# Kernel tuning notes

Hardware: AMD Instinct MI355X
Metric: run time of the kernel (lower is better)

## Reference

```python
import jax, jax.numpy as jnp
import numpy as np

N, E, F, H, A = 100000, 1600000, 256, 32, 64


def setup_inputs() -> dict:
    key = jax.random.key(0)
    ks = jax.random.split(key, 14)
    s = lambda k, shp, scale: (jax.random.normal(k, shp, dtype=jnp.float32) * scale)
    return {
        "features": jax.random.normal(ks[0], (N, F), dtype=jnp.float32),
        "edge_index": jax.random.randint(ks[1], (2, E), 0, N, dtype=jnp.int64),
        "W1": s(ks[2], (F, H), 1.0 / np.sqrt(F)), "b1": jnp.zeros((H,), jnp.float32),
        "W2": s(ks[3], (H, H), 1.0 / np.sqrt(H)), "b2": jnp.zeros((H,), jnp.float32),
        "pW1": s(ks[4], (H, 512), 1.0 / np.sqrt(H)), "pb1": jnp.zeros((512,), jnp.float32),
        "pW2": s(ks[5], (512, A), 1.0 / np.sqrt(512)), "pb2": jnp.zeros((A,), jnp.float32),
        "vW1": s(ks[6], (H, 512), 1.0 / np.sqrt(H)), "vb1": jnp.zeros((512,), jnp.float32),
        "vW2": s(ks[7], (512, 1), 1.0 / np.sqrt(512)), "vb2": jnp.zeros((1,), jnp.float32),
    }


def _gcn_conv(x, src, dst, W, b, n):
    # PyG GCNConv: x' = D^{-1/2} (A+I) D^{-1/2} (x W) + b  (self-loops already in src/dst)
    x = x @ W  # [n, out]
    deg = jax.ops.segment_sum(jnp.ones(src.shape[0], x.dtype), dst, num_segments=n)
    dinv = jnp.where(deg > 0, jax.lax.rsqrt(jnp.maximum(deg, 1e-12)), 0.0).astype(x.dtype)
    norm = dinv[src] * dinv[dst]                       # [E+n]
    msg = x[src] * norm[:, None]                       # gather + scale
    return jax.ops.segment_sum(msg, dst, num_segments=n) + b  # scatter-add


def reference(features, edge_index, W1, b1, W2, b2, pW1, pb1, pW2, pb2, vW1, vb1, vW2, vb2):
    n = features.shape[0]
    loop = jnp.arange(n, dtype=edge_index.dtype)
    src = jnp.concatenate([edge_index[0], loop])
    dst = jnp.concatenate([edge_index[1], loop])
    h = jax.nn.relu(_gcn_conv(features, src, dst, W1, b1, n))
    h = jax.nn.relu(_gcn_conv(h, src, dst, W2, b2, n))  # [n, H] == conv_out
    policy = jax.nn.relu(h @ pW1 + pb1) @ pW2 + pb2     # [n, A]
    value = jax.nn.relu(h @ vW1 + vb1) @ vW2 + vb2      # [n, 1]
    return policy, value
```

## Files before the change

### kernel.cpp

```cpp
#include <hip/hip_runtime.h>

#define FDIM 256
#define HDIM 32
#define D1   512
#define ADIM 64
#define BKT_SHIFT 9
#define BKT_NODES 512
#define CAP 12288

typedef __bf16 bf16x8 __attribute__((ext_vector_type(8)));
typedef float  f32x4  __attribute__((ext_vector_type(4)));

__device__ __forceinline__ float bf2f(unsigned short h){
  unsigned int u = ((unsigned int)h) << 16;
  return __builtin_bit_cast(float, u);
}
__device__ __forceinline__ unsigned short f2bf(float f){
  unsigned int u = __builtin_bit_cast(unsigned int, f);
  u = u + 0x7fff + ((u >> 16) & 1u);
  return (unsigned short)(u >> 16);
}
__device__ __forceinline__ unsigned int pk2(float a, float b){
  unsigned int ua = __builtin_bit_cast(unsigned int, a) + 0x8000u;
  unsigned int ub = __builtin_bit_cast(unsigned int, b) + 0x8000u;
  return (ua >> 16) | (ub & 0xffff0000u);
}

__global__ void k_zero(int* bkcur){
  bkcur[threadIdx.x] = 0;
}

__global__ __launch_bounds__(256) void k_stage(const int* __restrict__ src,
                                               const int* __restrict__ dst,
                                               int* __restrict__ bkcur,
                                               uint2* __restrict__ stage, int e){
  __shared__ int h[256], base[256], cur[256];
  int t = threadIdx.x;
  h[t] = 0; cur[t] = 0;
  __syncthreads();
  int lo = blockIdx.x*8192, hi = min(e, lo + 8192);
  for (int i = lo + t; i < hi; i += 256)
    atomicAdd(&h[dst[i] >> BKT_SHIFT], 1);
  __syncthreads();
  if (h[t] > 0) base[t] = t*CAP + atomicAdd(&bkcur[t], h[t]);
  __syncthreads();
  for (int i = lo + t; i < hi; i += 256){
    int d = dst[i]; int b = d >> BKT_SHIFT;
    int r = atomicAdd(&cur[b], 1);
    int idx = base[b] + r;
    if (idx < (b+1)*CAP)
      stage[idx] = make_uint2((unsigned)src[i], (unsigned)d);
  }
}

__global__ __launch_bounds__(256) void k_fine(const uint2* __restrict__ stage,
                                              const int* __restrict__ bkcur,
                                              int* __restrict__ rowptr,
                                              int* __restrict__ rowend,
                                              int* __restrict__ col,
                                              float* __restrict__ dinv, int n){
  __shared__ int h[512], ofs[512], s[256];
  int b = blockIdx.x, t = threadIdx.x;
  int e0 = b*CAP;
  int cnt = min(bkcur[b], CAP);
  int nb0 = b << BKT_SHIFT;
  h[t] = 0; h[t+256] = 0; __syncthreads();
  for (int i = e0 + t; i < e0 + cnt; i += 256)
    atomicAdd(&h[(int)stage[i].y - nb0], 1);
  __syncthreads();
  int a0 = h[2*t], a1 = h[2*t+1];
  int p0 = (a0 + 7) & ~7, p1 = (a1 + 7) & ~7;
  int v = p0 + p1;
  s[t] = v; __syncthreads();
  for (int off = 1; off < 256; off <<= 1){
    int tv = (t >= off) ? s[t-off] : 0; __syncthreads();
    s[t] += tv; __syncthreads();
  }
  int ex = s[t] - v;
  ofs[2*t] = ex; ofs[2*t+1] = ex + p0;
  int node0 = nb0 + 2*t, node1 = node0 + 1;
  if (node0 < n){
    rowptr[node0] = e0 + ex;       rowend[node0] = e0 + ex + p0;
    dinv[node0] = rsqrtf((float)(a0 + 1));
  }
  if (node1 < n){
    rowptr[node1] = e0 + ex + p0;  rowend[node1] = e0 + ex + p0 + p1;
    dinv[node1] = rsqrtf((float)(a1 + 1));
  }
  __syncthreads();
  for (int i = e0 + t; i < e0 + cnt; i += 256){
    uint2 u = stage[i];
    int r = atomicAdd(&ofs[(int)u.y - nb0], 1);
    col[e0 + r] = (int)u.x;
  }
  __syncthreads();
  {
    int st0 = ofs[2*t];
    for (int j = st0; j < ex + p0; ++j) col[e0 + j] = n;
    int st1 = ofs[2*t+1];
    for (int j = st1; j < ex + p0 + p1; ++j) col[e0 + j] = n;
  }
}

__device__ __forceinline__ void prep_one(int i, const float* __restrict__ src,
                                         unsigned short* __restrict__ dst,
                                         int nnt, int ld, int ncols){
  int j = i & 7; int L = (i >> 3) & 63; int t = i >> 9;
  int nt = t % nnt; int kb = t / nnt;
  int k = kb*32 + ((L >> 4) * 8) + j;
  int n = nt*16 + (L & 15);
  float v = (n < ncols) ? src[k*ld + n] : 0.f;
  dst[i] = f2bf(v);
}

__global__ void k_prep(const float* W1, const float* W2, const float* pW1,
                       const float* vW1, const float* pW2,
                       unsigned short* W1P, unsigned short* W2P, unsigned short* pW1P,
                       unsigned short* vW1P, unsigned short* pW2P){
  int i = blockIdx.x*256 + threadIdx.x;
  if (i < 8192) { prep_one(i, W1,  W1P,  2, 32, 32);   return; } i -= 8192;
  if (i < 1024) { prep_one(i, W2,  W2P,  2, 32, 32);   return; } i -= 1024;
  if (i < 16384){ prep_one(i, pW1, pW1P, 32, 512, 512); return; } i -= 16384;
  if (i < 16384){ prep_one(i, vW1, vW1P, 32, 512, 512); return; } i -= 16384;
  if (i < 32768){ prep_one(i, pW2, pW2P, 4, 64, 64);   return; }
}

__global__ __launch_bounds__(256) void k_gemm1(const float* __restrict__ feat,
                                               const unsigned short* __restrict__ W1P,
                                               const float* __restrict__ dinv,
                                               unsigned short* __restrict__ x1, int n){
  int lane = threadIdx.x & 63; int wv = threadIdx.x >> 6;
  int lid = lane & 15, quad = lane >> 4;
  int base = (blockIdx.x*4 + wv) * 16;
  int row = base + lid; if (row >= n) row = n - 1;
  const float* fr = feat + (size_t)row * FDIM;
  f32x4 acc0 = {0.f,0.f,0.f,0.f}, acc1 = {0.f,0.f,0.f,0.f};
#pragma unroll
  for (int kb = 0; kb < 8; ++kb){
    float4 fa = *(const float4*)(fr + kb*32 + quad*8);
    float4 fb = *(const float4*)(fr + kb*32 + quad*8 + 4);
    bf16x8 bfr;
    bfr[0]=(__bf16)fa.x; bfr[1]=(__bf16)fa.y; bfr[2]=(__bf16)fa.z; bfr[3]=(__bf16)fa.w;
    bfr[4]=(__bf16)fb.x; bfr[5]=(__bf16)fb.y; bfr[6]=(__bf16)fb.z; bfr[7]=(__bf16)fb.w;
    bf16x8 w0 = *(const bf16x8*)(W1P + (size_t)((kb*2+0)*64 + lane)*8);
    bf16x8 w1 = *(const bf16x8*)(W1P + (size_t)((kb*2+1)*64 + lane)*8);
    acc0 = __builtin_amdgcn_mfma_f32_16x16x32_bf16(w0, bfr, acc0, 0,0,0);
    acc1 = __builtin_amdgcn_mfma_f32_16x16x32_bf16(w1, bfr, acc1, 0,0,0);
  }
  int orow = base + lid;
  if (orow <= n){
    float di = (orow < n) ? dinv[orow] : 0.f;
    unsigned short* o = x1 + (size_t)orow*HDIM;
    uint2 q0, q1;
    q0.x = f2bf(acc0[0]*di) | ((unsigned)f2bf(acc0[1]*di)<<16);
    q0.y = f2bf(acc0[2]*di) | ((unsigned)f2bf(acc0[3]*di)<<16);
    q1.x = f2bf(acc1[0]*di) | ((unsigned)f2bf(acc1[1]*di)<<16);
    q1.y = f2bf(acc1[2]*di) | ((unsigned)f2bf(acc1[3]*di)<<16);
    *(uint2*)(o + quad*4)      = q0;
    *(uint2*)(o + 16 + quad*4) = q1;
  }
}

__global__ __launch_bounds__(256) void k_conv(const unsigned short* __restrict__ x,
                                              const float* __restrict__ dinv,
                                              const int* __restrict__ rowptr,
                                              const int* __restrict__ rowend,
                                              const int* __restrict__ col,
                                              const float* __restrict__ bias,
                                              unsigned short* __restrict__ y, int n){
  int node = (blockIdx.x*256 + threadIdx.x) >> 6;
  if (node >= n) return;
  int lane = threadIdx.x & 63;
  int c = lane & 31, eh = lane >> 5;
  float acc = (eh == 0) ? bf2f(x[(size_t)node*HDIM + c]) : 0.f;
  int rp = rowptr[node], re = rowend[node];
  int nb8 = (re - rp) >> 3;
  int jb = rp + (eh << 2);
#pragma clang loop unroll_count(2)
  for (int t = 0; t < nb8; ++t, jb += 8){
    int c0 = col[jb+0], c1 = col[jb+1], c2 = col[jb+2], c3 = col[jb+3];
    float v0 = bf2f(x[(size_t)c0*HDIM + c]);
    float v1 = bf2f(x[(size_t)c1*HDIM + c]);
    float v2 = bf2f(x[(size_t)c2*HDIM + c]);
    float v3 = bf2f(x[(size_t)c3*HDIM + c]);
    acc += (v0 + v1) + (v2 + v3);
  }
  acc += __shfl_xor(acc, 32);
  if (eh == 0){
    float v = acc * dinv[node] + bias[c];
    y[(size_t)node*HDIM + c] = f2bf(fmaxf(v, 0.f));
  }
}

__global__ __launch_bounds__(256) void k_gemm2(const unsigned short* __restrict__ h1,
                                               const unsigned short* __restrict__ W2P,
                                               const float* __restrict__ dinv,
                                               unsigned short* __restrict__ x2, int n){
  int lane = threadIdx.x & 63; int wv = threadIdx.x >> 6;
  int lid = lane & 15, quad = lane >> 4;
  int base = (blockIdx.x*4 + wv) * 16;
  int row = base + lid; if (row >= n) row = n - 1;
  bf16x8 hb = *(const bf16x8*)(h1 + (size_t)row*HDIM + quad*8);
  bf16x8 w0 = *(const bf16x8*)(W2P + (size_t)(0*64 + lane)*8);
  bf16x8 w1 = *(const bf16x8*)(W2P + (size_t)(1*64 + lane)*8);
  f32x4 z = {0.f,0.f,0.f,0.f};
  f32x4 a0 = __builtin_amdgcn_mfma_f32_16x16x32_bf16(w0, hb, z, 0,0,0);
  f32x4 a1 = __builtin_amdgcn_mfma_f32_16x16x32_bf16(w1, hb, z, 0,0,0);
  int orow = base + lid;
  if (orow <= n){
    float di = (orow < n) ? dinv[orow] : 0.f;
    unsigned short* o = x2 + (size_t)orow*HDIM;
    uint2 q0, q1;
    q0.x = f2bf(a0[0]*di) | ((unsigned)f2bf(a0[1]*di)<<16);
    q0.y = f2bf(a0[2]*di) | ((unsigned)f2bf(a0[3]*di)<<16);
    q1.x = f2bf(a1[0]*di) | ((unsigned)f2bf(a1[1]*di)<<16);
    q1.y = f2bf(a1[2]*di) | ((unsigned)f2bf(a1[3]*di)<<16);
    *(uint2*)(o + quad*4)      = q0;
    *(uint2*)(o + 16 + quad*4) = q1;
  }
}

#define TSTR 56
__global__ __launch_bounds__(256, 4) void k_head(const unsigned short* __restrict__ h,
    const unsigned short* __restrict__ pW1P, const unsigned short* __restrict__ pW2P,
    const unsigned short* __restrict__ vW1P, const float* __restrict__ vW2,
    const float* __restrict__ pb1, const float* __restrict__ pb2,
    const float* __restrict__ vb1, const float* __restrict__ vb2,
    float* __restrict__ pol, float* __restrict__ val, int n){
  __shared__ unsigned short lds[4*2*16*TSTR];
  int lane = threadIdx.x & 63; int wv = threadIdx.x >> 6;
  int lid = lane & 15, quad = lane >> 4;
  int nbase = (blockIdx.x*4 + wv) * 32;
  unsigned short* tb0 = lds + wv*(2*16*TSTR);
  unsigned short* tb1 = tb0 + 16*TSTR;
  int r0 = nbase + lid;      if (r0 >= n) r0 = n - 1;
  int r1 = nbase + 16 + lid; if (r1 >= n) r1 = n - 1;
  bf16x8 hf0 = *(const bf16x8*)(h + (size_t)r0*HDIM + quad*8);
  bf16x8 hf1 = *(const bf16x8*)(h + (size_t)r1*HDIM + quad*8);
  f32x4 z = {0.f,0.f,0.f,0.f};
  f32x4 acc[8] = {z,z,z,z,z,z,z,z};

#pragma unroll 2
  for (int kb = 0; kb < 16; ++kb){
    bf16x8 w0 = *(const bf16x8*)(pW1P + (size_t)((2*kb+0)*64 + lane)*8);
    bf16x8 w1 = *(const bf16x8*)(pW1P + (size_t)((2*kb+1)*64 + lane)*8);
    f32x4 c00 = __builtin_amdgcn_mfma_f32_16x16x32_bf16(w0, hf0, z, 0,0,0);
    f32x4 c01 = __builtin_amdgcn_mfma_f32_16x16x32_bf16(w1, hf0, z, 0,0,0);
    f32x4 c10 = __builtin_amdgcn_mfma_f32_16x16x32_bf16(w0, hf1, z, 0,0,0);
    f32x4 c11 = __builtin_amdgcn_mfma_f32_16x16x32_bf16(w1, hf1, z, 0,0,0);
    float4 b0 = *(const float4*)(pb1 + (2*kb+0)*16 + quad*4);
    float4 b1 = *(const float4*)(pb1 + (2*kb+1)*16 + quad*4);
    uint2 q;
    q.x = pk2(fmaxf(c00[0]+b0.x,0.f), fmaxf(c00[1]+b0.y,0.f));
    q.y = pk2(fmaxf(c00[2]+b0.z,0.f), fmaxf(c00[3]+b0.w,0.f));
    *(uint2*)(tb0 + lid*TSTR + quad*4) = q;
    q.x = pk2(fmaxf(c01[0]+b1.x,0.f), fmaxf(c01[1]+b1.y,0.f));
    q.y = pk2(fmaxf(c01[2]+b1.z,0.f), fmaxf(c01[3]+b1.w,0.f));
    *(uint2*)(tb0 + lid*TSTR + 16 + quad*4) = q;
    q.x = pk2(fmaxf(c10[0]+b0.x,0.f), fmaxf(c10[1]+b0.y,0.f));
    q.y = pk2(fmaxf(c10[2]+b0.z,0.f), fmaxf(c10[3]+b0.w,0.f));
    *(uint2*)(tb1 + lid*TSTR + quad*4) = q;
    q.x = pk2(fmaxf(c11[0]+b1.x,0.f), fmaxf(c11[1]+b1.y,0.f));
    q.y = pk2(fmaxf(c11[2]+b1.z,0.f), fmaxf(c11[3]+b1.w,0.f));
    *(uint2*)(tb1 + lid*TSTR + 16 + quad*4) = q;
    bf16x8 a0 = *(const bf16x8*)(tb0 + lid*TSTR + quad*8);
    bf16x8 a1 = *(const bf16x8*)(tb1 + lid*TSTR + quad*8);
#pragma unroll
    for (int tt = 0; tt < 4; ++tt){
      bf16x8 b = *(const bf16x8*)(pW2P + (size_t)((kb*4+tt)*64 + lane)*8);
      acc[tt]   = __builtin_amdgcn_mfma_f32_16x16x32_bf16(a0, b, acc[tt],   0,0,0);
      acc[4+tt] = __builtin_amdgcn_mfma_f32_16x16x32_bf16(a1, b, acc[4+tt], 0,0,0);
    }
  }
#pragma unroll
  for (int g = 0; g < 2; ++g){
#pragma unroll
    for (int tt = 0; tt < 4; ++tt){
      float pb2v = pb2[tt*16 + lid];
#pragma unroll
      for (int r = 0; r < 4; ++r){
        int node = nbase + g*16 + quad*4 + r;
        if (node < n) pol[(size_t)node*ADIM + tt*16 + lid] = acc[g*4+tt][r] + pb2v;
      }
    }
  }

  float va0 = 0.f, va1 = 0.f;
#pragma unroll 4
  for (int t = 0; t < 32; ++t){
    bf16x8 a = *(const bf16x8*)(vW1P + (size_t)(t*64 + lane)*8);
    f32x4 c0 = __builtin_amdgcn_mfma_f32_16x16x32_bf16(a, hf0, z, 0,0,0);
    f32x4 c1 = __builtin_amdgcn_mfma_f32_16x16x32_bf16(a, hf1, z, 0,0,0);
    float4 b  = *(const float4*)(vb1 + t*16 + quad*4);
    float4 w2 = *(const float4*)(vW2 + t*16 + quad*4);
    va0 += fmaxf(c0[0]+b.x,0.f)*w2.x + fmaxf(c0[1]+b.y,0.f)*w2.y
         + fmaxf(c0[2]+b.z,0.f)*w2.z + fmaxf(c0[3]+b.w,0.f)*w2.w;
    va1 += fmaxf(c1[0]+b.x,0.f)*w2.x + fmaxf(c1[1]+b.y,0.f)*w2.y
         + fmaxf(c1[2]+b.z,0.f)*w2.z + fmaxf(c1[3]+b.w,0.f)*w2.w;
  }
  va0 += __shfl_xor(va0, 16); va0 += __shfl_xor(va0, 32);
  va1 += __shfl_xor(va1, 16); va1 += __shfl_xor(va1, 32);
  if (quad == 0){
    float vb = vb2[0];
    int n0 = nbase + lid, n1 = nbase + 16 + lid;
    if (n0 < n) val[n0] = va0 + vb;
    if (n1 < n) val[n1] = va1 + vb;
  }
}

extern "C" void kernel_launch(void* const* d_in, const int* in_sizes, int n_in,
                              void* d_out, int out_size, void* d_ws, size_t ws_size,
                              hipStream_t stream){
  const float* feat = (const float*)d_in[0];
  const int*   edge = (const int*)d_in[1];
  const float* W1  = (const float*)d_in[2];
  const float* b1  = (const float*)d_in[3];
  const float* W2  = (const float*)d_in[4];
  const float* b2  = (const float*)d_in[5];
  const float* pW1 = (const float*)d_in[6];
  const float* pb1 = (const float*)d_in[7];
  const float* pW2 = (const float*)d_in[8];
  const float* pb2 = (const float*)d_in[9];
  const float* vW1 = (const float*)d_in[10];
  const float* vb1 = (const float*)d_in[11];
  const float* vW2 = (const float*)d_in[12];
  const float* vb2 = (const float*)d_in[13];
  int n = in_sizes[0] / FDIM;
  int e = in_sizes[1] / 2;
  int nbk = (n + BKT_NODES - 1) >> BKT_SHIFT;

  char* w = (char*)d_ws;
  auto alloc = [&](size_t bytes)->char*{
    char* p = w; w += (bytes + 255) & ~(size_t)255; return p;
  };
  size_t nodebuf = (size_t)(n+1)*HDIM*2;
  size_t stagesz = (size_t)nbk*CAP*8;
  char* stagebuf = alloc(stagesz > 2*nodebuf ? stagesz : 2*nodebuf);
  uint2* stage = (uint2*)stagebuf;
  unsigned short* x1 = (unsigned short*)stagebuf;
  unsigned short* h1 = (unsigned short*)(stagebuf + nodebuf);
  int*   col    = (int*)  alloc((size_t)nbk*CAP*4);
  int*   rowptr = (int*)  alloc((size_t)n*4);
  int*   rowend = (int*)  alloc((size_t)n*4);
  float* dinv   = (float*)alloc((size_t)n*4);
  int*   bkcur  = (int*)  alloc(256*4);
  unsigned short* W1P  = (unsigned short*)alloc(8192*2);
  unsigned short* W2P  = (unsigned short*)alloc(1024*2);
  unsigned short* pW1P = (unsigned short*)alloc(16384*2);
  unsigned short* vW1P = (unsigned short*)alloc(16384*2);
  unsigned short* pW2P = (unsigned short*)alloc(32768*2);

  int gb  = (n + 63)/64;
  int hb2 = (n + 127)/128;

  k_zero <<<1, 256, 0, stream>>>(bkcur);
  k_stage<<<(e + 8191)/8192, 256, 0, stream>>>(edge, edge + e, bkcur, stage, e);
  k_fine <<<nbk, 256, 0, stream>>>(stage, bkcur, rowptr, rowend, col, dinv, n);
  k_prep <<<(74752 + 255)/256, 256, 0, stream>>>(W1, W2, pW1, vW1, pW2,
                                                 W1P, W2P, pW1P, vW1P, pW2P);
  k_gemm1<<<gb, 256, 0, stream>>>(feat, W1P, dinv, x1, n);
  k_conv <<<(n + 3)/4, 256, 0, stream>>>(x1, dinv, rowptr, rowend, col, b1, h1, n);
  k_gemm2<<<gb, 256, 0, stream>>>(h1, W2P, dinv, x1, n);
  k_conv <<<(n + 3)/4, 256, 0, stream>>>(x1, dinv, rowptr, rowend, col, b2, h1, n);
  float* pol = (float*)d_out;
  float* val = pol + (size_t)n*ADIM;
  k_head <<<hb2, 256, 0, stream>>>(h1, pW1P, pW2P, vW1P, vW2,
                                   pb1, pb2, vb1, vb2, pol, val, n);
}
```

Baseline: 370.4 us.

## Fuse W2 GEMM into first conv, pack staged edges, merge zero into prep

The second-layer dense transform (h1 @ W2, scaled by dinv) now runs inside the first aggregation kernel. W2 sits in LDS and each node's post-ReLU row goes through a small per-wave LDS dot product, so the separate MFMA gemm2 kernel and its h1 round-trip through global memory are gone. Staged edges are packed into one 32-bit word (local dst in the high bits, src in the low 17 bits), which halves staging traffic. The bucket-counter zeroing is folded into the weight-prep kernel to save a launch, and the row bounds are clamped to CAP. The risks are that the fused GEMM uses scalar FP32 FMAs instead of MFMA, adds an LDS barrier to each conv block, and the 17-bit packing limits src to fewer than 131072 nodes.

```diff
diff --git a/kernel.cpp b/kernel.cpp
--- a/kernel.cpp
+++ b/kernel.cpp
@@ -26,14 +26,34 @@
   return (ua >> 16) | (ub & 0xffff0000u);
 }
 
-__global__ void k_zero(int* bkcur){
-  bkcur[threadIdx.x] = 0;
+__device__ __forceinline__ void prep_one(int i, const float* __restrict__ src,
+                                         unsigned short* __restrict__ dst,
+                                         int nnt, int ld, int ncols){
+  int j = i & 7; int L = (i >> 3) & 63; int t = i >> 9;
+  int nt = t % nnt; int kb = t / nnt;
+  int k = kb*32 + ((L >> 4) * 8) + j;
+  int n = nt*16 + (L & 15);
+  float v = (n < ncols) ? src[k*ld + n] : 0.f;
+  dst[i] = f2bf(v);
+}
+
+__global__ void k_prep(const float* W1, const float* pW1, const float* vW1,
+                       const float* pW2,
+                       unsigned short* W1P, unsigned short* pW1P,
+                       unsigned short* vW1P, unsigned short* pW2P,
+                       int* bkcur){
+  int i = blockIdx.x*256 + threadIdx.x;
+  if (i < 256)  { bkcur[i] = 0;                          return; } i -= 256;
+  if (i < 8192) { prep_one(i, W1,  W1P,  2, 32, 32);     return; } i -= 8192;
+  if (i < 16384){ prep_one(i, pW1, pW1P, 32, 512, 512);  return; } i -= 16384;
+  if (i < 16384){ prep_one(i, vW1, vW1P, 32, 512, 512);  return; } i -= 16384;
+  if (i < 32768){ prep_one(i, pW2, pW2P, 4, 64, 64);     return; }
 }
 
 __global__ __launch_bounds__(256) void k_stage(const int* __restrict__ src,
                                                const int* __restrict__ dst,
                                                int* __restrict__ bkcur,
-                                               uint2* __restrict__ stage, int e){
+                                               unsigned int* __restrict__ stage, int e){
   __shared__ int h[256], base[256], cur[256];
   int t = threadIdx.x;
   h[t] = 0; cur[t] = 0;
@@ -49,11 +69,11 @@
     int r = atomicAdd(&cur[b], 1);
     int idx = base[b] + r;
     if (idx < (b+1)*CAP)
-      stage[idx] = make_uint2((unsigned)src[i], (unsigned)d);
-  }
-}
-
-__global__ __launch_bounds__(256) void k_fine(const uint2* __restrict__ stage,
+      stage[idx] = ((unsigned int)(d & (BKT_NODES-1)) << 17) | (unsigned int)src[i];
+  }
+}
+
+__global__ __launch_bounds__(256) void k_fine(const unsigned int* __restrict__ stage,
                                               const int* __restrict__ bkcur,
                                               int* __restrict__ rowptr,
                                               int* __restrict__ rowend,
@@ -66,7 +86,7 @@
   int nb0 = b << BKT_SHIFT;
   h[t] = 0; h[t+256] = 0; __syncthreads();
   for (int i = e0 + t; i < e0 + cnt; i += 256)
-    atomicAdd(&h[(int)stage[i].y - nb0], 1);
+    atomicAdd(&h[stage[i] >> 17], 1);
   __syncthreads();
   int a0 = h[2*t], a1 = h[2*t+1];
   int p0 = (a0 + 7) & ~7, p1 = (a1 + 7) & ~7;
@@ -80,49 +100,26 @@
   ofs[2*t] = ex; ofs[2*t+1] = ex + p0;
   int node0 = nb0 + 2*t, node1 = node0 + 1;
   if (node0 < n){
-    rowptr[node0] = e0 + ex;       rowend[node0] = e0 + ex + p0;
+    rowptr[node0] = e0 + ex;       rowend[node0] = e0 + min(ex + p0, CAP);
     dinv[node0] = rsqrtf((float)(a0 + 1));
   }
   if (node1 < n){
-    rowptr[node1] = e0 + ex + p0;  rowend[node1] = e0 + ex + p0 + p1;
+    rowptr[node1] = e0 + min(ex + p0, CAP);  rowend[node1] = e0 + min(ex + p0 + p1, CAP);
     dinv[node1] = rsqrtf((float)(a1 + 1));
   }
   __syncthreads();
   for (int i = e0 + t; i < e0 + cnt; i += 256){
-    uint2 u = stage[i];
-    int r = atomicAdd(&ofs[(int)u.y - nb0], 1);
-    col[e0 + r] = (int)u.x;
+    unsigned int u = stage[i];
+    int r = atomicAdd(&ofs[(int)(u >> 17)], 1);
+    if (r < CAP) col[e0 + r] = (int)(u & 0x1FFFF);
   }
   __syncthreads();
   {
     int st0 = ofs[2*t];
-    for (int j = st0; j < ex + p0; ++j) col[e0 + j] = n;
+    for (int j = st0; j < ex + p0 && j < CAP; ++j) col[e0 + j] = n;
     int st1 = ofs[2*t+1];
-    for (int j = st1; j < ex + p0 + p1; ++j) col[e0 + j] = n;
-  }
-}
-
-__device__ __forceinline__ void prep_one(int i, const float* __restrict__ src,
-                                         unsigned short* __restrict__ dst,
-                                         int nnt, int ld, int ncols){
-  int j = i & 7; int L = (i >> 3) & 63; int t = i >> 9;
-  int nt = t % nnt; int kb = t / nnt;
-  int k = kb*32 + ((L >> 4) * 8) + j;
-  int n = nt*16 + (L & 15);
-  float v = (n < ncols) ? src[k*ld + n] : 0.f;
-  dst[i] = f2bf(v);
-}
-
-__global__ void k_prep(const float* W1, const float* W2, const float* pW1,
-                       const float* vW1, const float* pW2,
-                       unsigned short* W1P, unsigned short* W2P, unsigned short* pW1P,
-                       unsigned short* vW1P, unsigned short* pW2P){
-  int i = blockIdx.x*256 + threadIdx.x;
-  if (i < 8192) { prep_one(i, W1,  W1P,  2, 32, 32);   return; } i -= 8192;
-  if (i < 1024) { prep_one(i, W2,  W2P,  2, 32, 32);   return; } i -= 1024;
-  if (i < 16384){ prep_one(i, pW1, pW1P, 32, 512, 512); return; } i -= 16384;
-  if (i < 16384){ prep_one(i, vW1, vW1P, 32, 512, 512); return; } i -= 16384;
-  if (i < 32768){ prep_one(i, pW2, pW2P, 4, 64, 64);   return; }
+    for (int j = st1; j < ex + p0 + p1 && j < CAP; ++j) col[e0 + j] = n;
+  }
 }
 
 __global__ __launch_bounds__(256) void k_gemm1(const float* __restrict__ feat,
@@ -161,23 +158,32 @@
   }
 }
 
+template<int FUSE_W2>
 __global__ __launch_bounds__(256) void k_conv(const unsigned short* __restrict__ x,
                                               const float* __restrict__ dinv,
                                               const int* __restrict__ rowptr,
                                               const int* __restrict__ rowend,
                                               const int* __restrict__ col,
                                               const float* __restrict__ bias,
+                                              const float* __restrict__ W2,
                                               unsigned short* __restrict__ y, int n){
-  int node = (blockIdx.x*256 + threadIdx.x) >> 6;
-  if (node >= n) return;
-  int lane = threadIdx.x & 63;
-  int c = lane & 31, eh = lane >> 5;
+  __shared__ float W2s[FUSE_W2 ? 1024 : 1];
+  __shared__ float yrow[4][32];
+  int t = threadIdx.x;
+  if (FUSE_W2){
+    for (int j = t; j < 1024; j += 256) W2s[j] = W2[j];
+    __syncthreads();
+  }
+  int gid = (blockIdx.x*256 + t) >> 6;
+  int node = (gid < n) ? gid : n - 1;
+  int lane = t & 63;
+  int c = lane & 31, eh = lane >> 5, wv = t >> 6;
   float acc = (eh == 0) ? bf2f(x[(size_t)node*HDIM + c]) : 0.f;
   int rp = rowptr[node], re = rowend[node];
   int nb8 = (re - rp) >> 3;
   int jb = rp + (eh << 2);
 #pragma clang loop unroll_count(2)
-  for (int t = 0; t < nb8; ++t, jb += 8){
+  for (int it = 0; it < nb8; ++it, jb += 8){
     int c0 = col[jb+0], c1 = col[jb+1], c2 = col[jb+2], c3 = col[jb+3];
     float v0 = bf2f(x[(size_t)c0*HDIM + c]);
     float v1 = bf2f(x[(size_t)c1*HDIM + c]);
@@ -186,37 +192,23 @@
     acc += (v0 + v1) + (v2 + v3);
   }
   acc += __shfl_xor(acc, 32);
-  if (eh == 0){
-    float v = acc * dinv[node] + bias[c];
-    y[(size_t)node*HDIM + c] = f2bf(fmaxf(v, 0.f));
-  }
-}
-
-__global__ __launch_bounds__(256) void k_gemm2(const unsigned short* __restrict__ h1,
-                                               const unsigned short* __restrict__ W2P,
-                                               const float* __restrict__ dinv,
-                                               unsigned short* __restrict__ x2, int n){
-  int lane = threadIdx.x & 63; int wv = threadIdx.x >> 6;
-  int lid = lane & 15, quad = lane >> 4;
-  int base = (blockIdx.x*4 + wv) * 16;
-  int row = base + lid; if (row >= n) row = n - 1;
-  bf16x8 hb = *(const bf16x8*)(h1 + (size_t)row*HDIM + quad*8);
-  bf16x8 w0 = *(const bf16x8*)(W2P + (size_t)(0*64 + lane)*8);
-  bf16x8 w1 = *(const bf16x8*)(W2P + (size_t)(1*64 + lane)*8);
-  f32x4 z = {0.f,0.f,0.f,0.f};
-  f32x4 a0 = __builtin_amdgcn_mfma_f32_16x16x32_bf16(w0, hb, z, 0,0,0);
-  f32x4 a1 = __builtin_amdgcn_mfma_f32_16x16x32_bf16(w1, hb, z, 0,0,0);
-  int orow = base + lid;
-  if (orow <= n){
-    float di = (orow < n) ? dinv[orow] : 0.f;
-    unsigned short* o = x2 + (size_t)orow*HDIM;
-    uint2 q0, q1;
-    q0.x = f2bf(a0[0]*di) | ((unsigned)f2bf(a0[1]*di)<<16);
-    q0.y = f2bf(a0[2]*di) | ((unsigned)f2bf(a0[3]*di)<<16);
-    q1.x = f2bf(a1[0]*di) | ((unsigned)f2bf(a1[1]*di)<<16);
-    q1.y = f2bf(a1[2]*di) | ((unsigned)f2bf(a1[3]*di)<<16);
-    *(uint2*)(o + quad*4)      = q0;
-    *(uint2*)(o + 16 + quad*4) = q1;
+  float di = dinv[node];
+  if (FUSE_W2){
+    if (eh == 0) yrow[wv][c] = fmaxf(acc * di + bias[c], 0.f);
+    float a = 0.f;
+#pragma unroll
+    for (int k = 0; k < 16; ++k){
+      int kk = eh*16 + k;
+      a += yrow[wv][kk] * W2s[kk*32 + c];
+    }
+    a += __shfl_xor(a, 32);
+    if (eh == 0 && gid < n)
+      y[(size_t)node*HDIM + c] = f2bf(a * di);
+  } else {
+    if (eh == 0 && gid < n){
+      float v = acc * di + bias[c];
+      y[(size_t)node*HDIM + c] = f2bf(fmaxf(v, 0.f));
+    }
   }
 }
 
@@ -334,18 +326,18 @@
     char* p = w; w += (bytes + 255) & ~(size_t)255; return p;
   };
   size_t nodebuf = (size_t)(n+1)*HDIM*2;
-  size_t stagesz = (size_t)nbk*CAP*8;
+  size_t stagesz = (size_t)nbk*CAP*4;
   char* stagebuf = alloc(stagesz > 2*nodebuf ? stagesz : 2*nodebuf);
-  uint2* stage = (uint2*)stagebuf;
+  unsigned int* stage = (unsigned int*)stagebuf;
   unsigned short* x1 = (unsigned short*)stagebuf;
-  unsigned short* h1 = (unsigned short*)(stagebuf + nodebuf);
+  unsigned short* x2 = (unsigned short*)(stagebuf + nodebuf);
+  unsigned short* hb = x1;
   int*   col    = (int*)  alloc((size_t)nbk*CAP*4);
   int*   rowptr = (int*)  alloc((size_t)n*4);
   int*   rowend = (int*)  alloc((size_t)n*4);
   float* dinv   = (float*)alloc((size_t)n*4);
   int*   bkcur  = (int*)  alloc(256*4);
   unsigned short* W1P  = (unsigned short*)alloc(8192*2);
-  unsigned short* W2P  = (unsigned short*)alloc(1024*2);
   unsigned short* pW1P = (unsigned short*)alloc(16384*2);
   unsigned short* vW1P = (unsigned short*)alloc(16384*2);
   unsigned short* pW2P = (unsigned short*)alloc(32768*2);
@@ -353,17 +345,15 @@
   int gb  = (n + 63)/64;
   int hb2 = (n + 127)/128;
 
-  k_zero <<<1, 256, 0, stream>>>(bkcur);
+  k_prep <<<(73984 + 255)/256, 256, 0, stream>>>(W1, pW1, vW1, pW2,
+                                                 W1P, pW1P, vW1P, pW2P, bkcur);
   k_stage<<<(e + 8191)/8192, 256, 0, stream>>>(edge, edge + e, bkcur, stage, e);
   k_fine <<<nbk, 256, 0, stream>>>(stage, bkcur, rowptr, rowend, col, dinv, n);
-  k_prep <<<(74752 + 255)/256, 256, 0, stream>>>(W1, W2, pW1, vW1, pW2,
-                                                 W1P, W2P, pW1P, vW1P, pW2P);
   k_gemm1<<<gb, 256, 0, stream>>>(feat, W1P, dinv, x1, n);
-  k_conv <<<(n + 3)/4, 256, 0, stream>>>(x1, dinv, rowptr, rowend, col, b1, h1, n);
-  k_gemm2<<<gb, 256, 0, stream>>>(h1, W2P, dinv, x1, n);
-  k_conv <<<(n + 3)/4, 256, 0, stream>>>(x1, dinv, rowptr, rowend, col, b2, h1, n);
+  k_conv<1><<<(n + 3)/4, 256, 0, stream>>>(x1, dinv, rowptr, rowend, col, b1, W2, x2, n);
+  k_conv<0><<<(n + 3)/4, 256, 0, stream>>>(x2, dinv, rowptr, rowend, col, b2, nullptr, hb, n);
   float* pol = (float*)d_out;
   float* val = pol + (size_t)n*ADIM;
-  k_head <<<hb2, 256, 0, stream>>>(h1, pW1P, pW2P, vW1P, vW2,
+  k_head <<<hb2, 256, 0, stream>>>(hb, pW1P, pW2P, vW1P, vW2,
                                    pb1, pb2, vb1, vb2, pol, val, n);
 }
```

Result: slower. 378.3 us (+2.1%).

## Pack staged edges into 32-bit words, shrink buckets, fold zeroing into prep

Applied to the files above, without the earlier changes.

Each staged edge entry now packs the local destination (8 bits) and the source id (17 bits) into one 32-bit word instead of a uint2. This halves stage-buffer traffic. Buckets shrink to 256 nodes, which doubles the k_fine block count and gives more parallelism. k_stage chunks fall to 2048 edges, so more blocks are launched, and the separate zero kernel is merged into k_prep, removing one launch. k_conv's unroll rises to 4. The packing relies on node ids fitting in 17 bits, and the smaller CAP increases the risk of overflow truncation on skewed degree distributions.

```diff
diff --git a/kernel.cpp b/kernel.cpp
--- a/kernel.cpp
+++ b/kernel.cpp
@@ -4,9 +4,9 @@
 #define HDIM 32
 #define D1   512
 #define ADIM 64
-#define BKT_SHIFT 9
-#define BKT_NODES 512
-#define CAP 12288
+#define BKT_SHIFT 8
+#define BKT_NODES 256
+#define CAP 7168
 
 typedef __bf16 bf16x8 __attribute__((ext_vector_type(8)));
 typedef float  f32x4  __attribute__((ext_vector_type(4)));
@@ -24,82 +24,6 @@
   unsigned int ua = __builtin_bit_cast(unsigned int, a) + 0x8000u;
   unsigned int ub = __builtin_bit_cast(unsigned int, b) + 0x8000u;
   return (ua >> 16) | (ub & 0xffff0000u);
-}
-
-__global__ void k_zero(int* bkcur){
-  bkcur[threadIdx.x] = 0;
-}
-
-__global__ __launch_bounds__(256) void k_stage(const int* __restrict__ src,
-                                               const int* __restrict__ dst,
-                                               int* __restrict__ bkcur,
-                                               uint2* __restrict__ stage, int e){
-  __shared__ int h[256], base[256], cur[256];
-  int t = threadIdx.x;
-  h[t] = 0; cur[t] = 0;
-  __syncthreads();
-  int lo = blockIdx.x*8192, hi = min(e, lo + 8192);
-  for (int i = lo + t; i < hi; i += 256)
-    atomicAdd(&h[dst[i] >> BKT_SHIFT], 1);
-  __syncthreads();
-  if (h[t] > 0) base[t] = t*CAP + atomicAdd(&bkcur[t], h[t]);
-  __syncthreads();
-  for (int i = lo + t; i < hi; i += 256){
-    int d = dst[i]; int b = d >> BKT_SHIFT;
-    int r = atomicAdd(&cur[b], 1);
-    int idx = base[b] + r;
-    if (idx < (b+1)*CAP)
-      stage[idx] = make_uint2((unsigned)src[i], (unsigned)d);
-  }
-}
-
-__global__ __launch_bounds__(256) void k_fine(const uint2* __restrict__ stage,
-                                              const int* __restrict__ bkcur,
-                                              int* __restrict__ rowptr,
-                                              int* __restrict__ rowend,
-                                              int* __restrict__ col,
-                                              float* __restrict__ dinv, int n){
-  __shared__ int h[512], ofs[512], s[256];
-  int b = blockIdx.x, t = threadIdx.x;
-  int e0 = b*CAP;
-  int cnt = min(bkcur[b], CAP);
-  int nb0 = b << BKT_SHIFT;
-  h[t] = 0; h[t+256] = 0; __syncthreads();
-  for (int i = e0 + t; i < e0 + cnt; i += 256)
-    atomicAdd(&h[(int)stage[i].y - nb0], 1);
-  __syncthreads();
-  int a0 = h[2*t], a1 = h[2*t+1];
-  int p0 = (a0 + 7) & ~7, p1 = (a1 + 7) & ~7;
-  int v = p0 + p1;
-  s[t] = v; __syncthreads();
-  for (int off = 1; off < 256; off <<= 1){
-    int tv = (t >= off) ? s[t-off] : 0; __syncthreads();
-    s[t] += tv; __syncthreads();
-  }
-  int ex = s[t] - v;
-  ofs[2*t] = ex; ofs[2*t+1] = ex + p0;
-  int node0 = nb0 + 2*t, node1 = node0 + 1;
-  if (node0 < n){
-    rowptr[node0] = e0 + ex;       rowend[node0] = e0 + ex + p0;
-    dinv[node0] = rsqrtf((float)(a0 + 1));
-  }
-  if (node1 < n){
-    rowptr[node1] = e0 + ex + p0;  rowend[node1] = e0 + ex + p0 + p1;
-    dinv[node1] = rsqrtf((float)(a1 + 1));
-  }
-  __syncthreads();
-  for (int i = e0 + t; i < e0 + cnt; i += 256){
-    uint2 u = stage[i];
-    int r = atomicAdd(&ofs[(int)u.y - nb0], 1);
-    col[e0 + r] = (int)u.x;
-  }
-  __syncthreads();
-  {
-    int st0 = ofs[2*t];
-    for (int j = st0; j < ex + p0; ++j) col[e0 + j] = n;
-    int st1 = ofs[2*t+1];
-    for (int j = st1; j < ex + p0 + p1; ++j) col[e0 + j] = n;
-  }
 }
 
 __device__ __forceinline__ void prep_one(int i, const float* __restrict__ src,
@@ -116,13 +40,83 @@
 __global__ void k_prep(const float* W1, const float* W2, const float* pW1,
                        const float* vW1, const float* pW2,
                        unsigned short* W1P, unsigned short* W2P, unsigned short* pW1P,
-                       unsigned short* vW1P, unsigned short* pW2P){
+                       unsigned short* vW1P, unsigned short* pW2P,
+                       int* bkcur){
   int i = blockIdx.x*256 + threadIdx.x;
-  if (i < 8192) { prep_one(i, W1,  W1P,  2, 32, 32);   return; } i -= 8192;
-  if (i < 1024) { prep_one(i, W2,  W2P,  2, 32, 32);   return; } i -= 1024;
-  if (i < 16384){ prep_one(i, pW1, pW1P, 32, 512, 512); return; } i -= 16384;
-  if (i < 16384){ prep_one(i, vW1, vW1P, 32, 512, 512); return; } i -= 16384;
-  if (i < 32768){ prep_one(i, pW2, pW2P, 4, 64, 64);   return; }
+  if (i < 512)  { bkcur[i] = 0;                          return; } i -= 512;
+  if (i < 8192) { prep_one(i, W1,  W1P,  2, 32, 32);     return; } i -= 8192;
+  if (i < 1024) { prep_one(i, W2,  W2P,  2, 32, 32);     return; } i -= 1024;
+  if (i < 16384){ prep_one(i, pW1, pW1P, 32, 512, 512);  return; } i -= 16384;
+  if (i < 16384){ prep_one(i, vW1, vW1P, 32, 512, 512);  return; } i -= 16384;
+  if (i < 32768){ prep_one(i, pW2, pW2P, 4, 64, 64);     return; }
+}
+
+__global__ __launch_bounds__(256) void k_stage(const int* __restrict__ src,
+                                               const int* __restrict__ dst,
+                                               int* __restrict__ bkcur,
+                                               unsigned int* __restrict__ stage,
+                                               int e, int nbk){
+  __shared__ int h[400], base[400], cur[400];
+  int t = threadIdx.x;
+  for (int b = t; b < nbk; b += 256){ h[b] = 0; cur[b] = 0; }
+  __syncthreads();
+  int lo = blockIdx.x*2048, hi = min(e, lo + 2048);
+  for (int i = lo + t; i < hi; i += 256)
+    atomicAdd(&h[dst[i] >> BKT_SHIFT], 1);
+  __syncthreads();
+  for (int b = t; b < nbk; b += 256)
+    if (h[b] > 0) base[b] = b*CAP + atomicAdd(&bkcur[b], h[b]);
+  __syncthreads();
+  for (int i = lo + t; i < hi; i += 256){
+    int d = dst[i]; int b = d >> BKT_SHIFT;
+    int r = atomicAdd(&cur[b], 1);
+    int idx = base[b] + r;
+    if (idx < (b+1)*CAP)
+      stage[idx] = ((unsigned int)(d & (BKT_NODES-1)) << 17) | (unsigned int)src[i];
+  }
+}
+
+__global__ __launch_bounds__(256) void k_fine(const unsigned int* __restrict__ stage,
+                                              const int* __restrict__ bkcur,
+                                              int* __restrict__ rowptr,
+                                              int* __restrict__ rowend,
+                                              int* __restrict__ col,
+                                              float* __restrict__ dinv, int n){
+  __shared__ int h[256], ofs[256], s[256];
+  int b = blockIdx.x, t = threadIdx.x;
+  int e0 = b*CAP;
+  int cnt = min(bkcur[b], CAP);
+  int nb0 = b << BKT_SHIFT;
+  h[t] = 0; __syncthreads();
+  for (int i = e0 + t; i < e0 + cnt; i += 256)
+    atomicAdd(&h[stage[i] >> 17], 1);
+  __syncthreads();
+  int a = h[t];
+  int p = (a + 7) & ~7;
+  s[t] = p; __syncthreads();
+  for (int off = 1; off < 256; off <<= 1){
+    int tv = (t >= off) ? s[t-off] : 0; __syncthreads();
+    s[t] += tv; __syncthreads();
+  }
+  int ex = s[t] - p;
+  ofs[t] = ex;
+  int node = nb0 + t;
+  if (node < n){
+    rowptr[node] = e0 + min(ex, CAP);
+    rowend[node] = e0 + min(ex + p, CAP);
+    dinv[node] = rsqrtf((float)(a + 1));
+  }
+  __syncthreads();
+  for (int i = e0 + t; i < e0 + cnt; i += 256){
+    unsigned int u = stage[i];
+    int r = atomicAdd(&ofs[(int)(u >> 17)], 1);
+    if (r < CAP) col[e0 + r] = (int)(u & 0x1FFFF);
+  }
+  __syncthreads();
+  {
+    int st = ofs[t];
+    for (int j = st; j < ex + p && j < CAP; ++j) col[e0 + j] = n;
+  }
 }
 
 __global__ __launch_bounds__(256) void k_gemm1(const float* __restrict__ feat,
@@ -176,8 +170,8 @@
   int rp = rowptr[node], re = rowend[node];
   int nb8 = (re - rp) >> 3;
   int jb = rp + (eh << 2);
-#pragma clang loop unroll_count(2)
-  for (int t = 0; t < nb8; ++t, jb += 8){
+#pragma clang loop unroll_count(4)
+  for (int it = 0; it < nb8; ++it, jb += 8){
     int c0 = col[jb+0], c1 = col[jb+1], c2 = col[jb+2], c3 = col[jb+3];
     float v0 = bf2f(x[(size_t)c0*HDIM + c]);
     float v1 = bf2f(x[(size_t)c1*HDIM + c]);
@@ -334,16 +328,16 @@
     char* p = w; w += (bytes + 255) & ~(size_t)255; return p;
   };
   size_t nodebuf = (size_t)(n+1)*HDIM*2;
-  size_t stagesz = (size_t)nbk*CAP*8;
+  size_t stagesz = (size_t)nbk*CAP*4;
   char* stagebuf = alloc(stagesz > 2*nodebuf ? stagesz : 2*nodebuf);
-  uint2* stage = (uint2*)stagebuf;
+  unsigned int* stage = (unsigned int*)stagebuf;
   unsigned short* x1 = (unsigned short*)stagebuf;
   unsigned short* h1 = (unsigned short*)(stagebuf + nodebuf);
   int*   col    = (int*)  alloc((size_t)nbk*CAP*4);
   int*   rowptr = (int*)  alloc((size_t)n*4);
   int*   rowend = (int*)  alloc((size_t)n*4);
   float* dinv   = (float*)alloc((size_t)n*4);
-  int*   bkcur  = (int*)  alloc(256*4);
+  int*   bkcur  = (int*)  alloc(512*4);
   unsigned short* W1P  = (unsigned short*)alloc(8192*2);
   unsigned short* W2P  = (unsigned short*)alloc(1024*2);
   unsigned short* pW1P = (unsigned short*)alloc(16384*2);
@@ -353,11 +347,10 @@
   int gb  = (n + 63)/64;
   int hb2 = (n + 127)/128;
 
-  k_zero <<<1, 256, 0, stream>>>(bkcur);
-  k_stage<<<(e + 8191)/8192, 256, 0, stream>>>(edge, edge + e, bkcur, stage, e);
+  k_prep <<<(75264 + 255)/256, 256, 0, stream>>>(W1, W2, pW1, vW1, pW2,
+                                                 W1P, W2P, pW1P, vW1P, pW2P, bkcur);
+  k_stage<<<(e + 2047)/2048, 256, 0, stream>>>(edge, edge + e, bkcur, stage, e, nbk);
   k_fine <<<nbk, 256, 0, stream>>>(stage, bkcur, rowptr, rowend, col, dinv, n);
-  k_prep <<<(74752 + 255)/256, 256, 0, stream>>>(W1, W2, pW1, vW1, pW2,
-                                                 W1P, W2P, pW1P, vW1P, pW2P);
   k_gemm1<<<gb, 256, 0, stream>>>(feat, W1P, dinv, x1, n);
   k_conv <<<(n + 3)/4, 256, 0, stream>>>(x1, dinv, rowptr, rowend, col, b1, h1, n);
   k_gemm2<<<gb, 256, 0, stream>>>(h1, W2P, dinv, x1, n);
```

After: 380.9 us. 2.8% more time.
